# Performance work log

Measured on AMD Instinct MI355X. Metric: run time of the kernel, lower is better.

## Reference

```python
import jax, jax.numpy as jnp
import numpy as np

TOP_K = 2  # standard top-2 MoE gating


def setup_inputs() -> dict:
    key = jax.random.key(0)
    k1, k2, k3, k4 = jax.random.split(key, 4)
    T, D, E = 8192, 1024, 8
    x = jax.random.normal(k1, (T, D), dtype=jnp.float32)
    Wg = jax.random.normal(k2, (D, E), dtype=jnp.float32) * (1.0 / np.sqrt(D))
    We = jax.random.normal(k3, (E, D, D), dtype=jnp.float32) * (1.0 / np.sqrt(D))
    be = jax.random.normal(k4, (E, D), dtype=jnp.float32) * 0.02
    return {"x": x, "Wg": Wg, "We": We, "be": be}


def reference(x, Wg, We, be):
    # x: [T, D]; Wg: [D, E]; We: [E, D, D]; be: [E, D]
    T = x.shape[0]
    logits = x @ Wg                          # [T, E]
    probs = jax.nn.softmax(logits, axis=-1)  # [T, E]
    top_v, top_i = jax.lax.top_k(probs, TOP_K)           # [T, K]
    top_v = top_v / jnp.sum(top_v, axis=-1, keepdims=True)
    # dense combine weights [T, E] (zero for non-selected experts)
    cw = jnp.zeros_like(probs).at[jnp.arange(T)[:, None], top_i].add(top_v)
    # per-expert GEMM over all tokens (E is small), then masked combine
    h = jnp.einsum('td,edf->etf', x, We) + be[:, None, :]  # [E, T, D]
    h = jax.nn.relu(h)
    y = jnp.einsum('te,etf->tf', cw, h)                    # [T, D]
    return y
```

## Files before the change

kernel.cpp:

```cpp
#include <hip/hip_runtime.h>

#define T_TOKENS 8192
#define DMODEL   1024
#define NEXP     8

#define BM 256
#define BN 256
#define BK 64
#define NSTEP (DMODEL / BK)

typedef float f32x4  __attribute__((ext_vector_type(4)));
typedef short short8 __attribute__((ext_vector_type(8)));

__device__ __forceinline__ unsigned short f32_to_bf16(float f) {
    unsigned int u = __builtin_bit_cast(unsigned int, f);
    unsigned int r = 0x7FFFu + ((u >> 16) & 1u);
    return (unsigned short)((u + r) >> 16);
}

__global__ __launch_bounds__(256)
void prep(const float* __restrict__ x, const float* __restrict__ Wg,
          const float* __restrict__ We,
          unsigned short* __restrict__ xb, unsigned short* __restrict__ wt,
          int* __restrict__ top_e, float* __restrict__ top_w) {
    __shared__ unsigned short tile[64][72];
    const int bid = blockIdx.x;

    if (bid < 2048) {
        const int wave = threadIdx.x >> 6;
        const int lane = threadIdx.x & 63;
        const int t = bid * 4 + wave;

        float lg[8];
        #pragma unroll
        for (int e = 0; e < 8; ++e) lg[e] = 0.0f;

        const float* xr = x + (size_t)t * DMODEL;
        unsigned short* xo = xb + (size_t)t * DMODEL;

        #pragma unroll
        for (int j = 0; j < 4; ++j) {
            const int d = j * 256 + lane * 4;
            float4 xv = *reinterpret_cast<const float4*>(xr + d);
            ushort4 o;
            o.x = f32_to_bf16(xv.x);
            o.y = f32_to_bf16(xv.y);
            o.z = f32_to_bf16(xv.z);
            o.w = f32_to_bf16(xv.w);
            *reinterpret_cast<ushort4*>(xo + d) = o;
            const float xs[4] = {xv.x, xv.y, xv.z, xv.w};
            #pragma unroll
            for (int c = 0; c < 4; ++c) {
                const float4 wlo = *reinterpret_cast<const float4*>(Wg + (size_t)(d + c) * 8);
                const float4 whi = *reinterpret_cast<const float4*>(Wg + (size_t)(d + c) * 8 + 4);
                lg[0] += xs[c] * wlo.x;  lg[1] += xs[c] * wlo.y;
                lg[2] += xs[c] * wlo.z;  lg[3] += xs[c] * wlo.w;
                lg[4] += xs[c] * whi.x;  lg[5] += xs[c] * whi.y;
                lg[6] += xs[c] * whi.z;  lg[7] += xs[c] * whi.w;
            }
        }
        #pragma unroll
        for (int off = 1; off < 64; off <<= 1) {
            #pragma unroll
            for (int e = 0; e < 8; ++e) lg[e] += __shfl_xor(lg[e], off);
        }

        if (lane == 0) {
            int i1 = 0; float v1 = lg[0];
            #pragma unroll
            for (int e = 1; e < 8; ++e) if (lg[e] > v1) { v1 = lg[e]; i1 = e; }
            int i2 = -1; float v2 = -1e30f;
            #pragma unroll
            for (int e = 0; e < 8; ++e) if (e != i1 && lg[e] > v2) { v2 = lg[e]; i2 = e; }
            const float w1 = 1.0f / (1.0f + __expf(v2 - v1));
            top_e[t] = i1 | (i2 << 4);
            top_w[t] = w1;
        }
    } else {
        const int idx = bid - 2048;
        const int e   = idx >> 8;
        const int rem = idx & 255;
        const int d0  = (rem >> 4) * 64;
        const int f0  = (rem & 15) * 64;
        const float* src = We + ((size_t)e * DMODEL + d0) * DMODEL + f0;
        #pragma unroll
        for (int j = 0; j < 4; ++j) {
            const int ix = j * 256 + threadIdx.x;
            const int dl = ix >> 4;
            const int fq = ix & 15;
            float4 v = *reinterpret_cast<const float4*>(src + (size_t)dl * DMODEL + fq * 4);
            tile[fq * 4 + 0][dl] = f32_to_bf16(v.x);
            tile[fq * 4 + 1][dl] = f32_to_bf16(v.y);
            tile[fq * 4 + 2][dl] = f32_to_bf16(v.z);
            tile[fq * 4 + 3][dl] = f32_to_bf16(v.w);
        }
        __syncthreads();
        unsigned short* dst = wt + ((size_t)e * DMODEL + f0) * DMODEL + d0;
        #pragma unroll
        for (int j = 0; j < 4; ++j) {
            const int ix = j * 256 + threadIdx.x;
            const int fl = ix >> 4;
            const int dq = ix & 15;
            ushort4 v = *reinterpret_cast<const ushort4*>(&tile[fl][dq * 4]);
            *reinterpret_cast<ushort4*>(dst + (size_t)fl * DMODEL + dq * 4) = v;
        }
    }
}

__global__ __launch_bounds__(256)
void compact(const int* __restrict__ top_e, const float* __restrict__ top_w,
             int* __restrict__ counts, int* __restrict__ toks,
             float* __restrict__ wgts, int* __restrict__ rows) {
    const int e    = blockIdx.x;
    const int c    = blockIdx.y;
    const int tid  = threadIdx.x;
    const int wave = tid >> 6;
    const int lane = tid & 63;

    __shared__ int sm[256];
    __shared__ int red[4];
    __shared__ int ws[4];

    int mc = 0;
    const int4* tp = reinterpret_cast<const int4*>(top_e) + tid * 8;
    #pragma unroll
    for (int i = 0; i < 8; ++i) {
        int4 v = tp[i];
        mc += (((v.x & 15) == e) || (((v.x >> 4) & 15) == e)) ? 1 : 0;
        mc += (((v.y & 15) == e) || (((v.y >> 4) & 15) == e)) ? 1 : 0;
        mc += (((v.z & 15) == e) || (((v.z >> 4) & 15) == e)) ? 1 : 0;
        mc += (((v.w & 15) == e) || (((v.w >> 4) & 15) == e)) ? 1 : 0;
    }
    sm[tid] = mc;
    __syncthreads();

    int v = (tid < c * 8) ? sm[tid] : 0;
    #pragma unroll
    for (int off = 1; off < 64; off <<= 1) v += __shfl_xor(v, off);
    if (lane == 0) red[wave] = v;
    __syncthreads();
    const int base = red[0] + red[1] + red[2] + red[3];

    const int t  = c * 256 + tid;
    const int te = top_e[t];
    const int e1 = te & 15;
    const int e2 = (te >> 4) & 15;
    const bool m = (e1 == e) || (e2 == e);
    const unsigned long long b = __ballot(m);
    const int pos_in_wave = __popcll(b & ((1ull << lane) - 1ull));
    if (lane == 0) ws[wave] = __popcll(b);
    __syncthreads();

    int woff = base;
    #pragma unroll
    for (int i = 0; i < 4; ++i) if (i < wave) woff += ws[i];

    if (m) {
        const int pos = woff + pos_in_wave;
        const float w1 = top_w[t];
        toks[e * T_TOKENS + pos] = t;
        wgts[e * T_TOKENS + pos] = (e1 == e) ? w1 : 1.0f - w1;
        rows[t * 2 + ((e1 == e) ? 0 : 1)] = e * T_TOKENS + pos;
    }
    if (c == 31 && tid == 0)
        counts[e] = base + ws[0] + ws[1] + ws[2] + ws[3];
}

__global__ __launch_bounds__(512, 2)
void expert_gemm(const unsigned short* __restrict__ xb,
                 const unsigned short* __restrict__ wt,
                 const float* __restrict__ be,
                 const int* __restrict__ counts,
                 const int* __restrict__ toks,
                 const float* __restrict__ wgts,
                 unsigned short* __restrict__ hpart) {
    const int flat = blockIdx.x + 32 * (blockIdx.y + 4 * blockIdx.z);
    const int e    = flat & 7;
    const int rest = flat >> 3;
    const int fy   = rest & 3;
    const int tx   = rest >> 2;

    const int cnt = counts[e];
    const int p0  = tx * BM;
    if (p0 >= cnt) return;
    const int f0  = fy * BN;

    __shared__ unsigned short lds_w[BN * BK];
    __shared__ unsigned short lds_x[BM * BK];
    __shared__ int   tok_s[BM];
    __shared__ float wgt_s[BM];

    const int tid  = threadIdx.x;
    const int wave = tid >> 6;
    const int lane = tid & 63;

    if (tid < BM) {
        int p = p0 + tid;
        if (p < cnt) {
            tok_s[tid] = toks[e * T_TOKENS + p];
            wgt_s[tid] = wgts[e * T_TOKENS + p];
        } else {
            tok_s[tid] = 0;
            wgt_s[tid] = 0.0f;
        }
    }
    __syncthreads();

    const char* wsrc[4];
    const char* xsrc[4];
    #pragma unroll
    for (int s = 0; s < 4; ++s) {
        const int q    = wave * 4 + s;
        const int row  = q * 8 + (lane >> 3);
        const int scol = ((lane & 7) << 4) ^ ((row & 7) << 4);
        wsrc[s] = (const char*)wt + ((size_t)(e * DMODEL + f0 + row) * DMODEL) * 2 + scol;
        xsrc[s] = (const char*)xb + ((size_t)tok_s[row] * DMODEL) * 2 + scol;
    }

    f32x4 acc[8][4] = {};

    const int wm = wave >> 2;
    const int wn = wave & 3;
    const int wf = wm * 128;
    const int wp = wn * 64;

    #pragma unroll 1
    for (int t = 0; t < NSTEP; ++t) {
        const size_t ko = (size_t)t * BK * 2;
        #pragma unroll
        for (int s = 0; s < 4; ++s) {
            __builtin_amdgcn_global_load_lds(
                (const __attribute__((address_space(1))) void*)(wsrc[s] + ko),
                (__attribute__((address_space(3))) void*)((char*)lds_w + (wave * 4 + s) * 1024),
                16, 0, 0);
            __builtin_amdgcn_global_load_lds(
                (const __attribute__((address_space(1))) void*)(xsrc[s] + ko),
                (__attribute__((address_space(3))) void*)((char*)lds_x + (wave * 4 + s) * 1024),
                16, 0, 0);
        }
        __syncthreads();

        #pragma unroll
        for (int kk = 0; kk < 2; ++kk) {
            short8 afr[8], bfr[4];
            #pragma unroll
            for (int mi = 0; mi < 8; ++mi) {
                const int row = wf + mi * 16 + (lane & 15);
                const int kb  = (kk * 64 + ((lane >> 4) << 4)) ^ ((row & 7) << 4);
                afr[mi] = *(const short8*)((const char*)lds_w + row * 128 + kb);
            }
            #pragma unroll
            for (int ni = 0; ni < 4; ++ni) {
                const int row = wp + ni * 16 + (lane & 15);
                const int kb  = (kk * 64 + ((lane >> 4) << 4)) ^ ((row & 7) << 4);
                bfr[ni] = *(const short8*)((const char*)lds_x + row * 128 + kb);
            }
            #pragma unroll
            for (int mi = 0; mi < 8; ++mi)
                #pragma unroll
                for (int ni = 0; ni < 4; ++ni)
                    asm("v_mfma_f32_16x16x32_bf16 %0, %1, %2, %0"
                        : "+v"(acc[mi][ni])
                        : "v"(afr[mi]), "v"(bfr[ni]));
        }
        __syncthreads();
    }

    #pragma unroll
    for (int ni = 0; ni < 4; ++ni) {
        const int pl = wp + ni * 16 + (lane & 15);
        const int p  = p0 + pl;
        if (p >= cnt) continue;
        const float w = wgt_s[pl];
        unsigned short* hr = hpart + (size_t)(e * T_TOKENS + p) * DMODEL + f0 + wf;
        #pragma unroll
        for (int mi = 0; mi < 8; ++mi) {
            const int fb = mi * 16 + ((lane >> 4) << 2);
            const float* ber = be + (size_t)e * DMODEL + f0 + wf + fb;
            ushort4 o;
            float v0 = acc[mi][ni][0] + ber[0]; v0 = v0 > 0.f ? v0 : 0.f;
            float v1 = acc[mi][ni][1] + ber[1]; v1 = v1 > 0.f ? v1 : 0.f;
            float v2 = acc[mi][ni][2] + ber[2]; v2 = v2 > 0.f ? v2 : 0.f;
            float v3 = acc[mi][ni][3] + ber[3]; v3 = v3 > 0.f ? v3 : 0.f;
            o.x = f32_to_bf16(v0 * w);
            o.y = f32_to_bf16(v1 * w);
            o.z = f32_to_bf16(v2 * w);
            o.w = f32_to_bf16(v3 * w);
            *reinterpret_cast<ushort4*>(hr + fb) = o;
        }
    }
}

__global__ __launch_bounds__(256)
void combine(const unsigned short* __restrict__ hpart,
             const int* __restrict__ rows,
             float* __restrict__ y) {
    const int t = blockIdx.x;
    const int r0 = rows[t * 2 + 0];
    const int r1 = rows[t * 2 + 1];
    const int f = threadIdx.x * 4;
    ushort4 a = *reinterpret_cast<const ushort4*>(hpart + (size_t)r0 * DMODEL + f);
    ushort4 b = *reinterpret_cast<const ushort4*>(hpart + (size_t)r1 * DMODEL + f);
    float4 o;
    o.x = __builtin_bit_cast(float, (unsigned)a.x << 16) + __builtin_bit_cast(float, (unsigned)b.x << 16);
    o.y = __builtin_bit_cast(float, (unsigned)a.y << 16) + __builtin_bit_cast(float, (unsigned)b.y << 16);
    o.z = __builtin_bit_cast(float, (unsigned)a.z << 16) + __builtin_bit_cast(float, (unsigned)b.z << 16);
    o.w = __builtin_bit_cast(float, (unsigned)a.w << 16) + __builtin_bit_cast(float, (unsigned)b.w << 16);
    *reinterpret_cast<float4*>(y + (size_t)t * DMODEL + f) = o;
}

extern "C" void kernel_launch(void* const* d_in, const int* in_sizes, int n_in,
                              void* d_out, int out_size, void* d_ws, size_t ws_size,
                              hipStream_t stream) {
    (void)in_sizes; (void)n_in; (void)out_size; (void)ws_size;
    const float* x  = (const float*)d_in[0];
    const float* Wg = (const float*)d_in[1];
    const float* We = (const float*)d_in[2];
    const float* be = (const float*)d_in[3];
    float* y = (float*)d_out;

    char* ws = (char*)d_ws;
    unsigned short* xb     = (unsigned short*)(ws);
    unsigned short* wt     = (unsigned short*)(ws + (16u << 20));
    size_t off = (32u << 20);
    int*   counts = (int*)(ws + off);    off += 1024;
    int*   toks   = (int*)(ws + off);    off += (size_t)NEXP * T_TOKENS * 4;
    float* wgts   = (float*)(ws + off);  off += (size_t)NEXP * T_TOKENS * 4;
    int*   rows   = (int*)(ws + off);    off += (size_t)T_TOKENS * 2 * 4;
    int*   top_e  = (int*)(ws + off);    off += (size_t)T_TOKENS * 4;
    float* top_w  = (float*)(ws + off);
    unsigned short* hpart = (unsigned short*)(ws + (34u << 20));

    prep<<<dim3(4096), 256, 0, stream>>>(x, Wg, We, xb, wt, top_e, top_w);
    compact<<<dim3(NEXP, 32), 256, 0, stream>>>(top_e, top_w, counts, toks, wgts, rows);
    expert_gemm<<<dim3(T_TOKENS / BM, DMODEL / BN, NEXP), 512, 0, stream>>>(
        xb, wt, be, counts, toks, wgts, hpart);
    combine<<<dim3(T_TOKENS), 256, 0, stream>>>(hpart, rows, y);
}
```

Baseline: 127.8 us.

## Double-buffer expert GEMM LDS tiles with split-K staged prefetch pipeline

Reworks the expert GEMM main loop so global-to-LDS loads are double-buffered. Each 64-wide K step is split into two 32-wide halves, and the next tiles are prefetched while the current ones feed the MFMAs. Full __syncthreads are replaced by explicit vmcnt waits plus s_barrier, and s_setprio is raised around the MFMA block. The LDS layout and swizzle change to 64-byte rows, so the LDS footprint doubles. Hand-tuned waitcnt counts and barrier placement risk data races if the counts are wrong.

```diff
diff --git a/kernel.cpp b/kernel.cpp
--- a/kernel.cpp
+++ b/kernel.cpp
@@ -7,7 +7,7 @@
 #define BM 256
 #define BN 256
 #define BK 64
-#define NSTEP (DMODEL / BK)
+#define NITER (DMODEL / BK)
 
 typedef float f32x4  __attribute__((ext_vector_type(4)));
 typedef short short8 __attribute__((ext_vector_type(8)));
@@ -185,8 +185,7 @@
     if (p0 >= cnt) return;
     const int f0  = fy * BN;
 
-    __shared__ unsigned short lds_w[BN * BK];
-    __shared__ unsigned short lds_x[BM * BK];
+    __shared__ unsigned short lds[2][2][2][256 * 32];
     __shared__ int   tok_s[BM];
     __shared__ float wgt_s[BM];
 
@@ -206,16 +205,29 @@
     }
     __syncthreads();
 
-    const char* wsrc[4];
-    const char* xsrc[4];
-    #pragma unroll
-    for (int s = 0; s < 4; ++s) {
-        const int q    = wave * 4 + s;
-        const int row  = q * 8 + (lane >> 3);
-        const int scol = ((lane & 7) << 4) ^ ((row & 7) << 4);
-        wsrc[s] = (const char*)wt + ((size_t)(e * DMODEL + f0 + row) * DMODEL) * 2 + scol;
-        xsrc[s] = (const char*)xb + ((size_t)tok_s[row] * DMODEL) * 2 + scol;
-    }
+    const char* asrc[2];
+    const char* bsrc[2];
+    #pragma unroll
+    for (int s = 0; s < 2; ++s) {
+        const int r   = (wave * 2 + s) * 16 + (lane >> 2);
+        const int col = ((lane & 3) << 4) ^ (((r >> 1) & 3) << 4);
+        asrc[s] = (const char*)wt + ((size_t)(e * DMODEL + f0 + r)) * 2048 + col;
+        bsrc[s] = (const char*)xb + ((size_t)tok_s[r]) * 2048 + col;
+    }
+
+    auto stage = [&](int buf, int kh, int kbyte) {
+        #pragma unroll
+        for (int s = 0; s < 2; ++s) {
+            __builtin_amdgcn_global_load_lds(
+                (const __attribute__((address_space(1))) void*)(asrc[s] + kbyte + kh * 64),
+                (__attribute__((address_space(3))) void*)((char*)&lds[buf][0][kh][0] + (wave * 2 + s) * 1024),
+                16, 0, 0);
+            __builtin_amdgcn_global_load_lds(
+                (const __attribute__((address_space(1))) void*)(bsrc[s] + kbyte + kh * 64),
+                (__attribute__((address_space(3))) void*)((char*)&lds[buf][1][kh][0] + (wave * 2 + s) * 1024),
+                16, 0, 0);
+        }
+    };
 
     f32x4 acc[8][4] = {};
 
@@ -224,46 +236,54 @@
     const int wf = wm * 128;
     const int wp = wn * 64;
 
+    auto phase = [&](int buf, int kh) {
+        short8 afr[8], bfr[4];
+        const char* Ab = (const char*)&lds[buf][0][kh][0];
+        const char* Bb = (const char*)&lds[buf][1][kh][0];
+        #pragma unroll
+        for (int mi = 0; mi < 8; ++mi) {
+            const int row = wf + mi * 16 + (lane & 15);
+            afr[mi] = *(const short8*)(Ab + row * 64 +
+                        ((((lane >> 4)) << 4) ^ (((row >> 1) & 3) << 4)));
+        }
+        #pragma unroll
+        for (int ni = 0; ni < 4; ++ni) {
+            const int row = wp + ni * 16 + (lane & 15);
+            bfr[ni] = *(const short8*)(Bb + row * 64 +
+                        ((((lane >> 4)) << 4) ^ (((row >> 1) & 3) << 4)));
+        }
+        __builtin_amdgcn_s_setprio(1);
+        #pragma unroll
+        for (int mi = 0; mi < 8; ++mi)
+            #pragma unroll
+            for (int ni = 0; ni < 4; ++ni)
+                asm("v_mfma_f32_16x16x32_bf16 %0, %1, %2, %0"
+                    : "+v"(acc[mi][ni])
+                    : "v"(afr[mi]), "v"(bfr[ni]));
+        __builtin_amdgcn_s_setprio(0);
+    };
+
+    stage(0, 0, 0);
+    stage(0, 1, 0);
+    stage(1, 0, 128);
+    stage(1, 1, 128);
+
     #pragma unroll 1
-    for (int t = 0; t < NSTEP; ++t) {
-        const size_t ko = (size_t)t * BK * 2;
-        #pragma unroll
-        for (int s = 0; s < 4; ++s) {
-            __builtin_amdgcn_global_load_lds(
-                (const __attribute__((address_space(1))) void*)(wsrc[s] + ko),
-                (__attribute__((address_space(3))) void*)((char*)lds_w + (wave * 4 + s) * 1024),
-                16, 0, 0);
-            __builtin_amdgcn_global_load_lds(
-                (const __attribute__((address_space(1))) void*)(xsrc[s] + ko),
-                (__attribute__((address_space(3))) void*)((char*)lds_x + (wave * 4 + s) * 1024),
-                16, 0, 0);
-        }
-        __syncthreads();
-
-        #pragma unroll
-        for (int kk = 0; kk < 2; ++kk) {
-            short8 afr[8], bfr[4];
-            #pragma unroll
-            for (int mi = 0; mi < 8; ++mi) {
-                const int row = wf + mi * 16 + (lane & 15);
-                const int kb  = (kk * 64 + ((lane >> 4) << 4)) ^ ((row & 7) << 4);
-                afr[mi] = *(const short8*)((const char*)lds_w + row * 128 + kb);
-            }
-            #pragma unroll
-            for (int ni = 0; ni < 4; ++ni) {
-                const int row = wp + ni * 16 + (lane & 15);
-                const int kb  = (kk * 64 + ((lane >> 4) << 4)) ^ ((row & 7) << 4);
-                bfr[ni] = *(const short8*)((const char*)lds_x + row * 128 + kb);
-            }
-            #pragma unroll
-            for (int mi = 0; mi < 8; ++mi)
-                #pragma unroll
-                for (int ni = 0; ni < 4; ++ni)
-                    asm("v_mfma_f32_16x16x32_bf16 %0, %1, %2, %0"
-                        : "+v"(acc[mi][ni])
-                        : "v"(afr[mi]), "v"(bfr[ni]));
-        }
-        __syncthreads();
+    for (int t = 0; t < NITER; ++t) {
+        const int b = t & 1;
+        if (t == 0) {
+            asm volatile("s_waitcnt vmcnt(8)" ::: "memory");
+        } else if (t == NITER - 1) {
+            asm volatile("s_waitcnt vmcnt(0)" ::: "memory");
+        } else {
+            asm volatile("s_waitcnt vmcnt(4)" ::: "memory");
+        }
+        asm volatile("s_barrier" ::: "memory");
+        if (t >= 1 && t <= NITER - 2) stage(b ^ 1, 1, (t + 1) * 128);
+        phase(b, 0);
+        asm volatile("s_barrier" ::: "memory");
+        if (t <= NITER - 3) stage(b, 0, (t + 2) * 128);
+        phase(b, 1);
     }
 
     #pragma unroll
```

Result: slower. 140.0 us (+9.6%).
